# Kernel tuning notes

Hardware: AMD Instinct MI355X
Metric: run time of the kernel (lower is better)

The kernel has to match this reference:

```python
import jax, jax.numpy as jnp
import numpy as np

B, C, S = 2, 256, 24          # batch, hidden_size (channels), cube side
N = S * S * S                 # input_size = number of tokens (13824)
NH = 4                        # num_heads
DH = C // NH                  # head dim
P = 64                        # proj_size (low-rank K/V)
G = C // 32                   # conv groups in MHCResBlock
EPS_LN = 1e-5


def _lrelu(z):
    return jnp.where(z >= 0, z, 0.01 * z)


def _inorm(z):
    # instance norm over spatial dim, per (batch, channel); z: [B,C,N]
    m = jnp.mean(z, axis=-1, keepdims=True)
    v = jnp.var(z, axis=-1, keepdims=True)
    return (z - m) * jax.lax.rsqrt(v + EPS_LN)


def _gconv(z, w, b):
    # grouped 1x1x1 conv as per-group channel matmul; z: [B,C,N], w: [G,cin_g,cout_g]
    g, cin_g, cout_g = w.shape
    zg = z.reshape(z.shape[0], g, cin_g, z.shape[-1])
    out = jnp.einsum('bgin,gio->bgon', zg, w).reshape(z.shape[0], g * cout_g, z.shape[-1])
    return out + b[None, :, None]


def _ln(z, g, b):
    m = jnp.mean(z, axis=-1, keepdims=True)
    v = jnp.var(z, axis=-1, keepdims=True)
    return (z - m) * jax.lax.rsqrt(v + EPS_LN) * g + b


def _forward(x, pos_embed, ln_g, ln_b, gamma, temperature2, w_qkv, w_e, b_e,
             w_pool, b_pool, w_fc1, w_fc2, w_out1, b_out1, w_out2, b_out2,
             w_conv1, b_conv1, w_conv2, b_conv2):
    b_, c_, h_, w_, d_ = x.shape
    n_ = h_ * w_ * d_
    xf = x.reshape(b_, c_, n_)                      # [B,C,N]

    # MHCResBlock (UnetResBlock with grouped 1x1x1 convs + instance norm + lrelu)
    hdd = _lrelu(_inorm(_gconv(xf, w_conv1, b_conv1)))
    hdd = _inorm(_gconv(hdd, w_conv2, b_conv2))
    xc = _lrelu(hdd + xf)                           # [B,C,N]

    # tokens + pos embed + shared LayerNorm
    xt = xf.transpose(0, 2, 1) + pos_embed          # [B,N,C]
    xct = xc.transpose(0, 2, 1) + pos_embed
    x_n = _ln(xt, ln_g, ln_b)
    xc_n = _ln(xct, ln_g, ln_b)

    # QKV
    qkv = (x_n @ w_qkv).reshape(b_, n_, 3, NH, DH).transpose(2, 0, 3, 1, 4)  # [3,B,h,N,d]
    q, k, v = qkv[0], qkv[1], qkv[2]                # [B,h,N,d]
    qT = q.transpose(0, 1, 3, 2)                    # [B,h,d,N]
    kT = k.transpose(0, 1, 3, 2)
    vT = v.transpose(0, 1, 3, 2)

    # shared low-rank projection E == F over token dim (pre-normalization, as in source)
    k_proj = kT @ w_e + b_e                         # [B,h,d,P]
    v_proj = vT @ w_e + b_e                         # [B,h,d,P]

    # L2-normalize q over token dim (torch F.normalize eps=1e-12)
    qn = qT / jnp.maximum(jnp.linalg.norm(qT, axis=-1, keepdims=True), 1e-12)

    # channel attention: pool over tokens -> gated MLP -> sigmoid gate
    pooled = (xc_n.transpose(0, 2, 1) @ w_pool + b_pool).transpose(0, 2, 1)  # [B,1,C]
    gate = jax.nn.sigmoid(jax.nn.relu(pooled @ w_fc1) @ w_fc2)               # [B,1,C]
    x_CA = xc_n * gate                              # [B,N,C] (dropout = identity, eval)

    # spatial attention with projected K/V and per-head temperature
    attn = jnp.einsum('bhdn,bhdp->bhnp', qn, k_proj) * temperature2          # [B,h,N,P]
    attn = jax.nn.softmax(attn, axis=-1)
    x_SA = jnp.einsum('bhnp,bhdp->bhnd', attn, v_proj)                        # [B,h,N,d]
    # faithful permute(0,3,1,2).reshape(B,N,C) scramble from the source
    x_SA = x_SA.transpose(0, 3, 1, 2).reshape(b_, n_, c_)

    x_SA = x_SA @ w_out1 + b_out1                   # [B,N,C/2]
    x_CA = x_CA @ w_out2 + b_out2                   # [B,N,C/2]
    x_att = jnp.concatenate([x_SA, x_CA], axis=-1)  # [B,N,C]
    out = x_n + gamma * x_att
    return out.reshape(b_, h_, w_, d_, c_).transpose(0, 4, 1, 2, 3)


def setup_inputs() -> dict:
    key = jax.random.key(0)
    ks = jax.random.split(key, 16)
    f = lambda k, shape, sc=0.02: jax.random.normal(k, shape, jnp.float32) * sc
    return {
        'x': jax.random.normal(ks[0], (B, C, S, S, S), jnp.float32),
        'pos_embed': f(ks[1], (1, N, C)),
        'ln_g': jnp.ones((C,), jnp.float32),
        'ln_b': jnp.zeros((C,), jnp.float32),
        'gamma': jnp.full((C,), 1e-6, jnp.float32),
        'temperature2': jnp.ones((NH, 1, 1), jnp.float32),
        'w_qkv': f(ks[2], (C, 3 * C)),
        'w_e': f(ks[3], (N, P), 0.01),
        'b_e': jnp.zeros((P,), jnp.float32),
        'w_pool': f(ks[4], (N, 1), 0.01),
        'b_pool': jnp.zeros((1,), jnp.float32),
        'w_fc1': f(ks[5], (C, DH)),
        'w_fc2': f(ks[6], (DH, C)),
        'w_out1': f(ks[7], (C, C // 2)),
        'b_out1': jnp.zeros((C // 2,), jnp.float32),
        'w_out2': f(ks[8], (C, C // 2)),
        'b_out2': jnp.zeros((C // 2,), jnp.float32),
        'w_conv1': f(ks[9], (G, 32, 32), 0.1),
        'b_conv1': jnp.zeros((C,), jnp.float32),
        'w_conv2': f(ks[10], (G, 32, 32), 0.1),
        'b_conv2': jnp.zeros((C,), jnp.float32),
    }


def reference(x, pos_embed, ln_g, ln_b, gamma, temperature2, w_qkv, w_e, b_e,
              w_pool, b_pool, w_fc1, w_fc2, w_out1, b_out1, w_out2, b_out2,
              w_conv1, b_conv1, w_conv2, b_conv2):
    return _forward(x, pos_embed, ln_g, ln_b, gamma, temperature2, w_qkv, w_e, b_e,
                    w_pool, b_pool, w_fc1, w_fc2, w_out1, b_out1, w_out2, b_out2,
                    w_conv1, b_conv1, w_conv2, b_conv2)
```

## Files before the change

### kernel.cpp

```cpp
#include <hip/hip_runtime.h>
#include <hip/hip_bf16.h>
#include <math.h>

#define Bn 2
#define Cn 256
#define Nn 13824
#define NHn 4
#define Pn 64
#define Gn 8
#define NCH 54

typedef __bf16 bf16x8 __attribute__((ext_vector_type(8)));
typedef unsigned short us8v __attribute__((ext_vector_type(8)));
typedef unsigned short us4v __attribute__((ext_vector_type(4)));
typedef float f32x4 __attribute__((ext_vector_type(4)));

__device__ __forceinline__ unsigned short f2bf(float f) {
  __hip_bfloat16 h = __float2bfloat16(f);
  return __builtin_bit_cast(unsigned short, h);
}
__device__ __forceinline__ float bf2f(unsigned short u) {
  return __builtin_bit_cast(float, ((unsigned)u) << 16);
}
__device__ __forceinline__ unsigned pk2(float a, float b) {
  return (unsigned)f2bf(a) | ((unsigned)f2bf(b) << 16);
}

__global__ __launch_bounds__(256) void k_transpose_pos(const float* __restrict__ pos,
                                                       float* __restrict__ posT) {
  __shared__ float tile[64][65];
  int n0 = blockIdx.x * 64;
  int c0 = blockIdx.y * 64;
  int tc = threadIdx.x & 63;
  int tr = threadIdx.x >> 6;
  #pragma unroll
  for (int k = 0; k < 16; k++) {
    int n = tr + k * 4;
    tile[n][tc] = pos[(size_t)(n0 + n) * Cn + c0 + tc];
  }
  __syncthreads();
  #pragma unroll
  for (int k = 0; k < 16; k++) {
    int c = tr + k * 4;
    posT[(size_t)(c0 + c) * Nn + n0 + tc] = tile[tc][c];
  }
}

__global__ __launch_bounds__(256) void k_wcvt(const float* __restrict__ wqkv,
                                              const float* __restrict__ w1,
                                              unsigned short* __restrict__ wqT,
                                              unsigned short* __restrict__ w1T) {
  int j = blockIdx.x, c = threadIdx.x;
  if (j < 256) wqT[(size_t)j * 256 + c] = f2bf(wqkv[(size_t)c * 768 + j]);
  else w1T[(size_t)(j - 256) * 256 + c] = f2bf(w1[(size_t)c * 128 + (j - 256)]);
}

__global__ __launch_bounds__(256) void k_wet(const float* __restrict__ we,
                                             unsigned short* __restrict__ weT) {
  __shared__ float tile[64][65];
  int n0 = blockIdx.x * 64;
  int tc = threadIdx.x & 63;
  int tr = threadIdx.x >> 6;
  #pragma unroll
  for (int k = 0; k < 16; k++) {
    int n = tr + k * 4;
    tile[n][tc] = we[(size_t)(n0 + n) * Pn + tc];
  }
  __syncthreads();
  #pragma unroll
  for (int k = 0; k < 16; k++) {
    int p = tr + k * 4;
    weT[(size_t)p * Nn + n0 + tc] = f2bf(tile[tc][p]);
  }
}

template <bool NORM>
__global__ __launch_bounds__(256) void k_gconv(const float* __restrict__ src,
                                               const float* __restrict__ wt,
                                               const float* __restrict__ bias,
                                               const float* __restrict__ stats,
                                               float* __restrict__ dst,
                                               float* __restrict__ statacc) {
  int chunk = blockIdx.x, g = blockIdx.y, b = blockIdx.z;
  int t = threadIdx.x;
  int n = chunk * 256 + t;
  __shared__ float ws_[32][32];
  __shared__ float ms[32], rs[32], bs[32];
  __shared__ float sred[4][32][2];
  #pragma unroll
  for (int i = 0; i < 4; i++) {
    int e = t + 256 * i;
    ws_[e >> 5][e & 31] = wt[g * 1024 + e];
  }
  if (t < 32) {
    bs[t] = bias[g * 32 + t];
    if (NORM) {
      ms[t] = stats[(b * Cn + g * 32 + t) * 2 + 0];
      rs[t] = stats[(b * Cn + g * 32 + t) * 2 + 1];
    }
  }
  __syncthreads();
  float in[32];
  const float* sp = src + ((size_t)b * Cn + g * 32) * Nn + n;
  #pragma unroll
  for (int i = 0; i < 32; i++) {
    float v = sp[(size_t)i * Nn];
    if (NORM) {
      v = (v - ms[i]) * rs[i];
      v = v >= 0.f ? v : 0.01f * v;
    }
    in[i] = v;
  }
  int w = t >> 6, lane = t & 63;
  float* dp = dst + ((size_t)b * Cn + g * 32) * Nn + n;
  #pragma unroll
  for (int o = 0; o < 32; o++) {
    float acc = bs[o];
    #pragma unroll
    for (int i = 0; i < 32; i++) acc = fmaf(in[i], ws_[i][o], acc);
    dp[(size_t)o * Nn] = acc;
    float a = acc, a2 = acc * acc;
    #pragma unroll
    for (int off = 1; off < 64; off <<= 1) {
      a += __shfl_xor(a, off);
      a2 += __shfl_xor(a2, off);
    }
    if (lane == 0) { sred[w][o][0] = a; sred[w][o][1] = a2; }
  }
  __syncthreads();
  if (t < 64) {
    int o = t & 31, st = t >> 5;
    float v = sred[0][o][st] + sred[1][o][st] + sred[2][o][st] + sred[3][o][st];
    atomicAdd(&statacc[(b * Cn + g * 32 + o) * 2 + st], v);
  }
}

__global__ __launch_bounds__(256) void k_statfin(const float* __restrict__ acc,
                                                 float* __restrict__ stats) {
  int r = blockIdx.x * 256 + threadIdx.x;
  float s = acc[r * 2], ss = acc[r * 2 + 1];
  float m = s * (1.f / Nn);
  float var = ss * (1.f / Nn) - m * m;
  stats[r * 2 + 0] = m;
  stats[r * 2 + 1] = rsqrtf(var + 1e-5f);
}

__global__ __launch_bounds__(256) void k_fused_ln(
    const float* __restrict__ x, const float* __restrict__ t3,
    const float* __restrict__ posT, const float* __restrict__ stats3,
    const float* __restrict__ g, const float* __restrict__ beta,
    const float* __restrict__ wpool,
    unsigned short* __restrict__ xnbf, unsigned short* __restrict__ xnTbf,
    unsigned short* __restrict__ xcnbf, float* __restrict__ pooledacc) {
  int b = blockIdx.y, n0 = blockIdx.x * 32;
  int t = threadIdx.x, tg = t & 7, cg = t >> 3;
  int tok4 = tg * 4;
  __shared__ float vbuf[32 * 256];
  __shared__ float v2buf[32 * 256];
  __shared__ float red[4][8][4][4];
  __shared__ float tms[32][4];
  __shared__ float gb[256], bb[256], s3m[256], s3r[256];
  __shared__ float wp[32];
  __shared__ unsigned short Tb[2][32][36];

  gb[t] = g[t]; bb[t] = beta[t];
  s3m[t] = stats3[(b * Cn + t) * 2 + 0];
  s3r[t] = stats3[(b * Cn + t) * 2 + 1];
  if (t < 32) wp[t] = wpool[n0 + t];
  __syncthreads();

  float s1[4] = {}, q1[4] = {}, s2[4] = {}, q2[4] = {};
  #pragma unroll
  for (int ci = 0; ci < 8; ci++) {
    int c = ci * 32 + cg;
    f32x4 xv = *(const f32x4*)(x + ((size_t)b * Cn + c) * Nn + n0 + tok4);
    f32x4 pv = *(const f32x4*)(posT + (size_t)c * Nn + n0 + tok4);
    f32x4 tv = *(const f32x4*)(t3 + ((size_t)b * Cn + c) * Nn + n0 + tok4);
    float m3 = s3m[c], r3 = s3r[c];
    #pragma unroll
    for (int j = 0; j < 4; j++) {
      float v = xv[j] + pv[j];
      vbuf[(ci * 4 + j) * 256 + t] = v;
      s1[j] += v; q1[j] += v * v;
      float xcv = (tv[j] - m3) * r3 + xv[j];
      xcv = xcv >= 0.f ? xcv : 0.01f * xcv;
      float v2 = xcv + pv[j];
      v2buf[(ci * 4 + j) * 256 + t] = v2;
      s2[j] += v2; q2[j] += v2 * v2;
    }
  }
  #pragma unroll
  for (int j = 0; j < 4; j++) {
    float a = s1[j], bq = q1[j], c2 = s2[j], d2 = q2[j];
    #pragma unroll
    for (int off = 8; off < 64; off <<= 1) {
      a += __shfl_xor(a, off);
      bq += __shfl_xor(bq, off);
      c2 += __shfl_xor(c2, off);
      d2 += __shfl_xor(d2, off);
    }
    if ((t & 63) < 8) {
      int w = t >> 6, tgg = t & 7;
      red[w][tgg][j][0] = a; red[w][tgg][j][1] = bq;
      red[w][tgg][j][2] = c2; red[w][tgg][j][3] = d2;
    }
  }
  __syncthreads();
  if (t < 32) {
    int tgg = t >> 2, j = t & 3;
    float a = 0, bq = 0, c2 = 0, d2 = 0;
    #pragma unroll
    for (int w = 0; w < 4; w++) {
      a += red[w][tgg][j][0]; bq += red[w][tgg][j][1];
      c2 += red[w][tgg][j][2]; d2 += red[w][tgg][j][3];
    }
    float m1 = a * (1.f / 256.f);
    float r1 = rsqrtf(bq * (1.f / 256.f) - m1 * m1 + 1e-5f);
    float m2 = c2 * (1.f / 256.f);
    float r2 = rsqrtf(d2 * (1.f / 256.f) - m2 * m2 + 1e-5f);
    tms[t][0] = m1; tms[t][1] = r1; tms[t][2] = m2; tms[t][3] = r2;
  }
  __syncthreads();
  float m1v[4], r1v[4], m2v[4], r2v[4];
  #pragma unroll
  for (int j = 0; j < 4; j++) {
    m1v[j] = tms[tok4 + j][0]; r1v[j] = tms[tok4 + j][1];
    m2v[j] = tms[tok4 + j][2]; r2v[j] = tms[tok4 + j][3];
  }
  int row = t >> 3, seg = t & 7;
  #pragma unroll
  for (int ci = 0; ci < 8; ci++) {
    int c = ci * 32 + cg;
    float gg = gb[c], bv = bb[c];
    us4v o4;
    #pragma unroll
    for (int j = 0; j < 4; j++) {
      float v = vbuf[(ci * 4 + j) * 256 + t];
      o4[j] = f2bf((v - m1v[j]) * r1v[j] * gg + bv);
    }
    *(us4v*)(xnTbf + ((size_t)b * Cn + c) * Nn + n0 + tok4) = o4;
    #pragma unroll
    for (int j = 0; j < 4; j++) Tb[ci & 1][tok4 + j][cg] = o4[j];
    __syncthreads();
    *(us4v*)(xnbf + ((size_t)b * Nn + n0 + row) * Cn + ci * 32 + seg * 4) =
        *(const us4v*)&Tb[ci & 1][row][seg * 4];
  }
  #pragma unroll
  for (int ci = 0; ci < 8; ci++) {
    int c = ci * 32 + cg;
    float gg = gb[c], bv = bb[c];
    us4v o4;
    float pp = 0.f;
    #pragma unroll
    for (int j = 0; j < 4; j++) {
      float v = v2buf[(ci * 4 + j) * 256 + t];
      float o = (v - m2v[j]) * r2v[j] * gg + bv;
      o4[j] = f2bf(o);
      pp = fmaf(o, wp[tok4 + j], pp);
    }
    #pragma unroll
    for (int j = 0; j < 4; j++) Tb[ci & 1][tok4 + j][cg] = o4[j];
    pp += __shfl_xor(pp, 1);
    pp += __shfl_xor(pp, 2);
    pp += __shfl_xor(pp, 4);
    __syncthreads();
    *(us4v*)(xcnbf + ((size_t)b * Nn + n0 + row) * Cn + ci * 32 + seg * 4) =
        *(const us4v*)&Tb[ci & 1][row][seg * 4];
    if (tg == 0) atomicAdd(&pooledacc[b * Cn + c], pp);
  }
}

__global__ __launch_bounds__(256) void k_gemm_q(
    const unsigned short* __restrict__ Aw,
    const unsigned short* __restrict__ Bx,
    unsigned short* __restrict__ qo,
    float* __restrict__ qsq) {
  __shared__ char lds[24576];
  int b = blockIdx.z, n0 = blockIdx.x * 128, j0 = blockIdx.y * 64;
  int t = threadIdx.x, lane = t & 63, wid = t >> 6;
  int wj = wid >> 1, wt = wid & 1;
  f32x4 acc[2][4];
  #pragma unroll
  for (int i = 0; i < 2; i++)
    #pragma unroll
    for (int j = 0; j < 4; j++) acc[i][j] = (f32x4){0.f, 0.f, 0.f, 0.f};
  for (int k0 = 0; k0 < 256; k0 += 64) {
    {
      int r = t >> 2, off = (t & 3) * 16;
      const unsigned short* ga = Aw + (size_t)(j0 + r) * 256 + k0 + off;
      #pragma unroll
      for (int i = 0; i < 2; i++)
        *(us8v*)(lds + r * 128 + ((off * 2 + 16 * i) ^ ((r & 7) << 4))) = *(const us8v*)(ga + i * 8);
      int rb = t >> 1, offb = (t & 1) * 32;
      const unsigned short* gb = Bx + ((size_t)b * Nn + n0 + rb) * 256 + k0 + offb;
      #pragma unroll
      for (int i = 0; i < 4; i++)
        *(us8v*)(lds + 8192 + rb * 128 + ((offb * 2 + 16 * i) ^ ((rb & 7) << 4))) = *(const us8v*)(gb + i * 8);
    }
    __syncthreads();
    #pragma unroll
    for (int ks = 0; ks < 2; ks++) {
      int kb = ks * 64 + (lane >> 4) * 16;
      bf16x8 af[2], bfr[4];
      #pragma unroll
      for (int mt = 0; mt < 2; mt++) {
        int row = wj * 32 + mt * 16 + (lane & 15);
        af[mt] = *(bf16x8*)(lds + row * 128 + (kb ^ ((row & 7) << 4)));
      }
      #pragma unroll
      for (int tt = 0; tt < 4; tt++) {
        int row = wt * 64 + tt * 16 + (lane & 15);
        bfr[tt] = *(bf16x8*)(lds + 8192 + row * 128 + (kb ^ ((row & 7) << 4)));
      }
      #pragma unroll
      for (int mt = 0; mt < 2; mt++)
        #pragma unroll
        for (int tt = 0; tt < 4; tt++)
          acc[mt][tt] = __builtin_amdgcn_mfma_f32_16x16x32_bf16(af[mt], bfr[tt], acc[mt][tt], 0, 0, 0);
    }
    __syncthreads();
  }
  #pragma unroll
  for (int mt = 0; mt < 2; mt++)
    #pragma unroll
    for (int r = 0; r < 4; r++) {
      float v = 0.f;
      #pragma unroll
      for (int tt = 0; tt < 4; tt++) { float e = acc[mt][tt][r]; v = fmaf(e, e, v); }
      #pragma unroll
      for (int m = 1; m < 16; m <<= 1) v += __shfl_xor(v, m);
      if ((lane & 15) == 0)
        atomicAdd(&qsq[b * Cn + j0 + wj * 32 + mt * 16 + (lane >> 4) * 4 + r], v);
    }
  unsigned short* O = (unsigned short*)lds;
  #pragma unroll
  for (int mt = 0; mt < 2; mt++)
    #pragma unroll
    for (int tt = 0; tt < 4; tt++) {
      int tok = wt * 64 + tt * 16 + (lane & 15);
      int jb = wj * 32 + mt * 16 + ((lane >> 4) << 2);
      uint2 v;
      v.x = pk2(acc[mt][tt][0], acc[mt][tt][1]);
      v.y = pk2(acc[mt][tt][2], acc[mt][tt][3]);
      *(uint2*)(O + tok * 72 + jb) = v;
    }
  __syncthreads();
  int tok = t >> 1, js = (t & 1) * 32;
  unsigned short* dst = qo + ((size_t)b * Nn + n0 + tok) * 256 + j0 + js;
  #pragma unroll
  for (int i = 0; i < 4; i++) *(us8v*)(dst + i * 8) = *(const us8v*)(O + tok * 72 + js + i * 8);
}

__global__ __launch_bounds__(256) void k_xe(const unsigned short* __restrict__ xnT,
                                            const unsigned short* __restrict__ weT,
                                            float* __restrict__ part) {
  __shared__ char lds[16384];
  int chunk = blockIdx.x, ct = blockIdx.y, b = blockIdx.z;
  int c0 = ct * 64, nb = chunk * 256;
  int t = threadIdx.x, lane = t & 63, wid = t >> 6;
  f32x4 acc4[4];
  #pragma unroll
  for (int i = 0; i < 4; i++) acc4[i] = (f32x4){0.f, 0.f, 0.f, 0.f};
  for (int k0 = 0; k0 < 256; k0 += 64) {
    int r = t >> 2, off = (t & 3) * 16;
    const unsigned short* ga = xnT + ((size_t)b * Cn + c0 + r) * Nn + nb + k0 + off;
    const unsigned short* gb = weT + (size_t)r * Nn + nb + k0 + off;
    #pragma unroll
    for (int i = 0; i < 2; i++) {
      *(us8v*)(lds + r * 128 + ((off * 2 + 16 * i) ^ ((r & 7) << 4))) = *(const us8v*)(ga + i * 8);
      *(us8v*)(lds + 8192 + r * 128 + ((off * 2 + 16 * i) ^ ((r & 7) << 4))) = *(const us8v*)(gb + i * 8);
    }
    __syncthreads();
    #pragma unroll
    for (int ks = 0; ks < 2; ks++) {
      int kb = ks * 64 + (lane >> 4) * 16;
      int rowa = wid * 16 + (lane & 15);
      bf16x8 a = *(bf16x8*)(lds + rowa * 128 + (kb ^ ((rowa & 7) << 4)));
      #pragma unroll
      for (int pt = 0; pt < 4; pt++) {
        int rowb = pt * 16 + (lane & 15);
        bf16x8 bv = *(bf16x8*)(lds + 8192 + rowb * 128 + (kb ^ ((rowb & 7) << 4)));
        acc4[pt] = __builtin_amdgcn_mfma_f32_16x16x32_bf16(a, bv, acc4[pt], 0, 0, 0);
      }
    }
    __syncthreads();
  }
  size_t base = ((size_t)(b * NCH + chunk)) * (Cn * Pn);
  #pragma unroll
  for (int pt = 0; pt < 4; pt++)
    #pragma unroll
    for (int r = 0; r < 4; r++) {
      int c = c0 + wid * 16 + (lane >> 4) * 4 + r;
      int p = pt * 16 + (lane & 15);
      part[base + (size_t)c * Pn + p] = acc4[pt][r];
    }
}

__global__ __launch_bounds__(256) void k_xe_reduce(const float* __restrict__ part,
                                                   float* __restrict__ xe) {
  int i = blockIdx.x * 256 + threadIdx.x;
  int b = i / (Cn * Pn);
  int cp = i % (Cn * Pn);
  float s = 0.f;
  for (int ch = 0; ch < NCH; ch++) s += part[(size_t)(b * NCH + ch) * Cn * Pn + cp];
  xe[i] = s;
}

__global__ __launch_bounds__(256) void k_kvproj(const float* __restrict__ xe,
                                                const float* __restrict__ wqkv,
                                                const float* __restrict__ be,
                                                const float* __restrict__ qsq,
                                                const float* __restrict__ temp,
                                                unsigned short* __restrict__ kvp) {
  int hd = blockIdx.x * 4 + (threadIdx.x >> 6);
  int kv = blockIdx.y, b = blockIdx.z;
  int p = threadIdx.x & 63;
  int col = (kv + 1) * Cn + hd;
  float acc = be[p];
  for (int c = 0; c < Cn; c++)
    acc = fmaf(xe[((size_t)b * Cn + c) * Pn + p], wqkv[(size_t)c * 768 + col], acc);
  int h = hd >> 6, d = hd & 63;
  if (kv == 0) {
    float sc = 1.f / fmaxf(sqrtf(qsq[b * Cn + hd]), 1e-12f);
    acc *= sc * temp[h];
    kvp[((size_t)(b * 4 + h)) * 4096 + p * 64 + d] = f2bf(acc);
  } else {
    kvp[32768 + ((size_t)(b * 4 + h)) * 4096 + d * 64 + p] = f2bf(acc);
  }
}

__global__ __launch_bounds__(256) void k_gate(const float* __restrict__ pooledacc,
                                              const float* __restrict__ bpool,
                                              const float* __restrict__ wfc1,
                                              const float* __restrict__ wfc2,
                                              float* __restrict__ gate) {
  int b = blockIdx.x, t = threadIdx.x;
  __shared__ float pl[256], h1[64];
  pl[t] = pooledacc[b * Cn + t] + bpool[0];
  __syncthreads();
  if (t < 64) {
    float a = 0.f;
    for (int c = 0; c < Cn; c++) a = fmaf(pl[c], wfc1[c * 64 + t], a);
    h1[t] = fmaxf(a, 0.f);
  }
  __syncthreads();
  float a = 0.f;
  for (int j = 0; j < 64; j++) a = fmaf(h1[j], wfc2[j * Cn + t], a);
  gate[b * Cn + t] = 1.f / (1.f + __expf(-a));
}

__global__ __launch_bounds__(256) void k_w2gT(const float* __restrict__ gate,
                                              const float* __restrict__ w2,
                                              unsigned short* __restrict__ w2gT) {
  int j = blockIdx.x, b = blockIdx.y, c = threadIdx.x;
  w2gT[((size_t)b * 128 + j) * 256 + c] = f2bf(gate[b * Cn + c] * w2[(size_t)c * 128 + j]);
}

__global__ __launch_bounds__(128) void k_attn(const unsigned short* __restrict__ qbf,
                                              const unsigned short* __restrict__ kvp,
                                              unsigned short* __restrict__ xsa) {
  __shared__ char lds[16384 + 2 * 9216];
  int nb = blockIdx.x, h = blockIdx.y, b = blockIdx.z;
  int t = threadIdx.x, lane = t & 63, w = t >> 6;
  char* kpT = lds;
  char* vp = lds + 8192;
  unsigned short* P = (unsigned short*)(lds + 16384 + w * 9216);
  const unsigned short* kg = kvp + ((size_t)(b * 4 + h)) * 4096;
  const unsigned short* vg = kvp + 32768 + ((size_t)(b * 4 + h)) * 4096;
  {
    int r = t >> 1, off = (t & 1) * 32;
    #pragma unroll
    for (int i = 0; i < 4; i++) {
      *(us8v*)(kpT + r * 128 + ((off * 2 + 16 * i) ^ ((r & 7) << 4))) = *(const us8v*)(kg + r * 64 + off + i * 8);
      *(us8v*)(vp + r * 128 + ((off * 2 + 16 * i) ^ ((r & 7) << 4))) = *(const us8v*)(vg + r * 64 + off + i * 8);
    }
  }
  __syncthreads();
  int n0 = nb * 128 + w * 64;
  bf16x8 qf[4][2];
  #pragma unroll
  for (int tt = 0; tt < 4; tt++)
    #pragma unroll
    for (int ks = 0; ks < 2; ks++) {
      int n = n0 + tt * 16 + (lane & 15);
      qf[tt][ks] = *(const bf16x8*)(qbf + ((size_t)b * Nn + n) * 256 + h * 64 + ks * 32 + (lane >> 4) * 8);
    }
  f32x4 s[4][4];
  #pragma unroll
  for (int i = 0; i < 4; i++)
    #pragma unroll
    for (int j = 0; j < 4; j++) s[i][j] = (f32x4){0.f, 0.f, 0.f, 0.f};
  #pragma unroll
  for (int ks = 0; ks < 2; ks++) {
    int kb = ks * 64 + (lane >> 4) * 16;
    #pragma unroll
    for (int mt = 0; mt < 4; mt++) {
      int row = mt * 16 + (lane & 15);
      bf16x8 a = *(bf16x8*)(kpT + row * 128 + (kb ^ ((row & 7) << 4)));
      #pragma unroll
      for (int tt = 0; tt < 4; tt++)
        s[mt][tt] = __builtin_amdgcn_mfma_f32_16x16x32_bf16(a, qf[tt][ks], s[mt][tt], 0, 0, 0);
    }
  }
  #pragma unroll
  for (int tt = 0; tt < 4; tt++) {
    float mx = -1e30f;
    #pragma unroll
    for (int mt = 0; mt < 4; mt++)
      #pragma unroll
      for (int r = 0; r < 4; r++) mx = fmaxf(mx, s[mt][tt][r]);
    mx = fmaxf(mx, __shfl_xor(mx, 16));
    mx = fmaxf(mx, __shfl_xor(mx, 32));
    float den = 0.f;
    #pragma unroll
    for (int mt = 0; mt < 4; mt++)
      #pragma unroll
      for (int r = 0; r < 4; r++) {
        float e = __expf(s[mt][tt][r] - mx);
        s[mt][tt][r] = e; den += e;
      }
    den += __shfl_xor(den, 16);
    den += __shfl_xor(den, 32);
    float inv = 1.f / den;
    #pragma unroll
    for (int mt = 0; mt < 4; mt++)
      #pragma unroll
      for (int r = 0; r < 4; r++) s[mt][tt][r] *= inv;
  }
  #pragma unroll
  for (int mt = 0; mt < 4; mt++)
    #pragma unroll
    for (int tt = 0; tt < 4; tt++) {
      int tok = tt * 16 + (lane & 15);
      int pb = mt * 16 + ((lane >> 4) << 2);
      uint2 v;
      v.x = pk2(s[mt][tt][0], s[mt][tt][1]);
      v.y = pk2(s[mt][tt][2], s[mt][tt][3]);
      *(uint2*)(P + tok * 72 + pb) = v;
    }
  bf16x8 pf[4][2];
  #pragma unroll
  for (int mt = 0; mt < 4; mt++)
    #pragma unroll
    for (int ks = 0; ks < 2; ks++)
      pf[mt][ks] = *(const bf16x8*)(P + (mt * 16 + (lane & 15)) * 72 + ks * 32 + (lane >> 4) * 8);
  f32x4 o[4][4];
  #pragma unroll
  for (int i = 0; i < 4; i++)
    #pragma unroll
    for (int j = 0; j < 4; j++) o[i][j] = (f32x4){0.f, 0.f, 0.f, 0.f};
  #pragma unroll
  for (int ks = 0; ks < 2; ks++) {
    int kb = ks * 64 + (lane >> 4) * 16;
    #pragma unroll
    for (int nt = 0; nt < 4; nt++) {
      int row = nt * 16 + (lane & 15);
      bf16x8 bfv = *(bf16x8*)(vp + row * 128 + (kb ^ ((row & 7) << 4)));
      #pragma unroll
      for (int mt = 0; mt < 4; mt++)
        o[mt][nt] = __builtin_amdgcn_mfma_f32_16x16x32_bf16(pf[mt][ks], bfv, o[mt][nt], 0, 0, 0);
    }
  }
  #pragma unroll
  for (int mt = 0; mt < 4; mt++)
    #pragma unroll
    for (int nt = 0; nt < 4; nt++) {
      int d = nt * 16 + (lane & 15);
      int tb = mt * 16 + ((lane >> 4) << 2);
      uint2 v;
      v.x = pk2(o[mt][nt][0], o[mt][nt][1]);
      v.y = pk2(o[mt][nt][2], o[mt][nt][3]);
      *(uint2*)(P + d * 72 + tb) = v;
    }
  size_t fb = (size_t)b * Cn * Nn + ((size_t)(lane * 4 + h)) * Nn + n0;
  #pragma unroll
  for (int k = 0; k < 8; k++)
    *(us8v*)(xsa + fb + k * 8) = *(const us8v*)(P + lane * 72 + k * 8);
}

__global__ __launch_bounds__(256) void k_gemm_out(
    const unsigned short* __restrict__ Aw, size_t a_bstride,
    const unsigned short* __restrict__ Bx,
    const float* __restrict__ bias, int cbase,
    const unsigned short* __restrict__ xnT, const float* __restrict__ gamma,
    float* __restrict__ outp) {
  __shared__ char lds[33792];
  int b = blockIdx.z, n0 = blockIdx.x * 128, j0 = blockIdx.y * 64;
  int t = threadIdx.x, lane = t & 63, wid = t >> 6;
  int wj = wid >> 1, wt = wid & 1;
  const unsigned short* Ab = Aw + a_bstride * b;
  f32x4 acc[2][4];
  #pragma unroll
  for (int i = 0; i < 2; i++)
    #pragma unroll
    for (int j = 0; j < 4; j++) acc[i][j] = (f32x4){0.f, 0.f, 0.f, 0.f};
  for (int k0 = 0; k0 < 256; k0 += 64) {
    {
      int r = t >> 2, off = (t & 3) * 16;
      const unsigned short* ga = Ab + (size_t)(j0 + r) * 256 + k0 + off;
      #pragma unroll
      for (int i = 0; i < 2; i++)
        *(us8v*)(lds + r * 128 + ((off * 2 + 16 * i) ^ ((r & 7) << 4))) = *(const us8v*)(ga + i * 8);
      int rb = t >> 1, offb = (t & 1) * 32;
      const unsigned short* gb = Bx + ((size_t)b * Nn + n0 + rb) * 256 + k0 + offb;
      #pragma unroll
      for (int i = 0; i < 4; i++)
        *(us8v*)(lds + 8192 + rb * 128 + ((offb * 2 + 16 * i) ^ ((rb & 7) << 4))) = *(const us8v*)(gb + i * 8);
    }
    __syncthreads();
    #pragma unroll
    for (int ks = 0; ks < 2; ks++) {
      int kb = ks * 64 + (lane >> 4) * 16;
      bf16x8 af[2], bfr[4];
      #pragma unroll
      for (int mt = 0; mt < 2; mt++) {
        int row = wj * 32 + mt * 16 + (lane & 15);
        af[mt] = *(bf16x8*)(lds + row * 128 + (kb ^ ((row & 7) << 4)));
      }
      #pragma unroll
      for (int tt = 0; tt < 4; tt++) {
        int row = wt * 64 + tt * 16 + (lane & 15);
        bfr[tt] = *(bf16x8*)(lds + 8192 + row * 128 + (kb ^ ((row & 7) << 4)));
      }
      #pragma unroll
      for (int mt = 0; mt < 2; mt++)
        #pragma unroll
        for (int tt = 0; tt < 4; tt++)
          acc[mt][tt] = __builtin_amdgcn_mfma_f32_16x16x32_bf16(af[mt], bfr[tt], acc[mt][tt], 0, 0, 0);
    }
    __syncthreads();
  }
  float* OT = (float*)lds;
  #pragma unroll
  for (int mt = 0; mt < 2; mt++)
    #pragma unroll
    for (int tt = 0; tt < 4; tt++)
      #pragma unroll
      for (int r = 0; r < 4; r++) {
        int j = wj * 32 + mt * 16 + (lane >> 4) * 4 + r;
        int tok = wt * 64 + tt * 16 + (lane & 15);
        OT[j * 132 + tok] = acc[mt][tt][r];
      }
  __syncthreads();
  int jj = t >> 2, ts = (t & 3) * 32;
  int c = cbase + j0 + jj;
  float gm = gamma[c], bi = bias[j0 + jj];
  const unsigned short* xn = xnT + ((size_t)b * Cn + c) * Nn + n0 + ts;
  float* op = outp + ((size_t)b * Cn + c) * Nn + n0 + ts;
  #pragma unroll
  for (int i = 0; i < 8; i++) {
    f32x4 v = *(const f32x4*)(&OT[jj * 132 + ts + i * 4]);
    us4v xv = *(const us4v*)(xn + i * 4);
    f32x4 ov;
    #pragma unroll
    for (int e = 0; e < 4; e++) ov[e] = bf2f(xv[e]) + gm * (v[e] + bi);
    *(f32x4*)(op + i * 4) = ov;
  }
}

extern "C" void kernel_launch(void* const* d_in, const int* in_sizes, int n_in,
                              void* d_out, int out_size, void* d_ws, size_t ws_size,
                              hipStream_t stream) {
  const float* x      = (const float*)d_in[0];
  const float* pos    = (const float*)d_in[1];
  const float* ln_g   = (const float*)d_in[2];
  const float* ln_b   = (const float*)d_in[3];
  const float* gamma  = (const float*)d_in[4];
  const float* temp2  = (const float*)d_in[5];
  const float* w_qkv  = (const float*)d_in[6];
  const float* w_e    = (const float*)d_in[7];
  const float* b_e    = (const float*)d_in[8];
  const float* w_pool = (const float*)d_in[9];
  const float* b_pool = (const float*)d_in[10];
  const float* w_fc1  = (const float*)d_in[11];
  const float* w_fc2  = (const float*)d_in[12];
  const float* w_out1 = (const float*)d_in[13];
  const float* b_out1 = (const float*)d_in[14];
  const float* w_out2 = (const float*)d_in[15];
  const float* b_out2 = (const float*)d_in[16];
  const float* w_c1   = (const float*)d_in[17];
  const float* b_c1   = (const float*)d_in[18];
  const float* w_c2   = (const float*)d_in[19];
  const float* b_c2   = (const float*)d_in[20];
  (void)in_sizes; (void)n_in; (void)out_size; (void)ws_size;
  float* out = (float*)d_out;

  const size_t SZ = (size_t)Bn * Cn * Nn;
  const size_t NC = (size_t)Nn * Cn;
  char* base = (char*)d_ws;
  size_t off = 0;
  auto alloc = [&](size_t bytes) { void* p = base + off; off += (bytes + 255) & ~(size_t)255; return p; };
  float* t3     = (float*)alloc(SZ * 4);
  char*  alias  = (char*)alloc(SZ * 4);
  float* posT   = (float*)alloc(NC * 4);
  float* xepart = (float*)alloc((size_t)NCH * Bn * Cn * Pn * 4);
  unsigned short* xnbf  = (unsigned short*)alloc(SZ * 2);
  unsigned short* xnTbf = (unsigned short*)alloc(SZ * 2);
  unsigned short* xcnbf = (unsigned short*)alloc(SZ * 2);
  unsigned short* weT   = (unsigned short*)alloc((size_t)Pn * Nn * 2);
  float* zeros  = (float*)alloc(3072 * 4);
  float* stats1acc = zeros;
  float* stats3acc = zeros + 1024;
  float* qsq       = zeros + 2048;
  float* pooledacc = zeros + 2560;
  float* stats1 = (float*)alloc(1024 * 4);
  float* stats3 = (float*)alloc(1024 * 4);
  float* xe     = (float*)alloc(32768 * 4);
  float* gateb  = (float*)alloc(512 * 4);
  unsigned short* kvp  = (unsigned short*)alloc(65536 * 2);
  unsigned short* w2gt = (unsigned short*)alloc(65536 * 2);
  unsigned short* wqT  = (unsigned short*)alloc(65536 * 2);
  unsigned short* w1T  = (unsigned short*)alloc(32768 * 2);

  float* t1 = (float*)alias;
  unsigned short* qbf   = (unsigned short*)alias;
  unsigned short* xsabf = (unsigned short*)alias + SZ;

  hipMemsetAsync(zeros, 0, 3072 * 4, stream);
  k_wcvt<<<dim3(384), 256, 0, stream>>>(w_qkv, w_out1, wqT, w1T);
  k_wet<<<dim3(216), 256, 0, stream>>>(w_e, weT);
  k_transpose_pos<<<dim3(216, 4), 256, 0, stream>>>(pos, posT);
  k_gconv<false><<<dim3(NCH, Gn, Bn), 256, 0, stream>>>(x, w_c1, b_c1, nullptr, t1, stats1acc);
  k_statfin<<<dim3(2), 256, 0, stream>>>(stats1acc, stats1);
  k_gconv<true><<<dim3(NCH, Gn, Bn), 256, 0, stream>>>(t1, w_c2, b_c2, stats1, t3, stats3acc);
  k_statfin<<<dim3(2), 256, 0, stream>>>(stats3acc, stats3);
  k_fused_ln<<<dim3(432, Bn), 256, 0, stream>>>(x, t3, posT, stats3, ln_g, ln_b, w_pool,
                                                xnbf, xnTbf, xcnbf, pooledacc);
  k_gemm_q<<<dim3(108, 4, Bn), 256, 0, stream>>>(wqT, xnbf, qbf, qsq);
  k_xe<<<dim3(NCH, 4, Bn), 256, 0, stream>>>(xnTbf, weT, xepart);
  k_xe_reduce<<<dim3(128), 256, 0, stream>>>(xepart, xe);
  k_kvproj<<<dim3(64, 2, Bn), 256, 0, stream>>>(xe, w_qkv, b_e, qsq, temp2, kvp);
  k_gate<<<dim3(Bn), 256, 0, stream>>>(pooledacc, b_pool, w_fc1, w_fc2, gateb);
  k_w2gT<<<dim3(128, Bn), 256, 0, stream>>>(gateb, w_out2, w2gt);
  k_attn<<<dim3(108, NHn, Bn), 128, 0, stream>>>(qbf, kvp, xsabf);
  k_gemm_out<<<dim3(108, 2, Bn), 256, 0, stream>>>(w1T, 0, xsabf, b_out1, 0, xnTbf, gamma, out);
  k_gemm_out<<<dim3(108, 2, Bn), 256, 0, stream>>>(w2gt, (size_t)128 * 256, xcnbf, b_out2, 128, xnTbf, gamma, out);
}
```

Baseline: 406.6 us.

## Move grouped convs to bf16 MFMA GEMMs on token-major layout and merge prep kernels

Replaces the scalar FP32 grouped 1x1x1 convolutions with a generic bf16 MFMA GEMM kernel that uses block-diagonal expanded weights on a token-major bf16 copy of x. Intermediates become bf16, and the instance-norm statistics are accumulated in the GEMM epilogue. All weight conversions, the input transpose and the zeroing are merged into a single prep kernel. LayerNorm is rewritten to read token-major bf16, a separate transpose produces xnT, and the gate is applied inside the output GEMM rather than prebuilt. This cuts FP32 memory traffic and launch count, at the cost of dense 256x256 matmuls that waste 7/8 of their FLOPs on zero blocks and lower-precision intermediates.

```diff
diff --git a/kernel.cpp b/kernel.cpp
--- a/kernel.cpp
+++ b/kernel.cpp
@@ -26,113 +26,235 @@
   return (unsigned)f2bf(a) | ((unsigned)f2bf(b) << 16);
 }
 
-__global__ __launch_bounds__(256) void k_transpose_pos(const float* __restrict__ pos,
-                                                       float* __restrict__ posT) {
-  __shared__ float tile[64][65];
-  int n0 = blockIdx.x * 64;
-  int c0 = blockIdx.y * 64;
-  int tc = threadIdx.x & 63;
-  int tr = threadIdx.x >> 6;
-  #pragma unroll
-  for (int k = 0; k < 16; k++) {
-    int n = tr + k * 4;
-    tile[n][tc] = pos[(size_t)(n0 + n) * Cn + c0 + tc];
-  }
-  __syncthreads();
-  #pragma unroll
-  for (int k = 0; k < 16; k++) {
-    int c = tr + k * 4;
-    posT[(size_t)(c0 + c) * Nn + n0 + tc] = tile[tc][c];
-  }
-}
-
-__global__ __launch_bounds__(256) void k_wcvt(const float* __restrict__ wqkv,
-                                              const float* __restrict__ w1,
-                                              unsigned short* __restrict__ wqT,
-                                              unsigned short* __restrict__ w1T) {
-  int j = blockIdx.x, c = threadIdx.x;
-  if (j < 256) wqT[(size_t)j * 256 + c] = f2bf(wqkv[(size_t)c * 768 + j]);
-  else w1T[(size_t)(j - 256) * 256 + c] = f2bf(w1[(size_t)c * 128 + (j - 256)]);
-}
-
-__global__ __launch_bounds__(256) void k_wet(const float* __restrict__ we,
-                                             unsigned short* __restrict__ weT) {
-  __shared__ float tile[64][65];
-  int n0 = blockIdx.x * 64;
-  int tc = threadIdx.x & 63;
-  int tr = threadIdx.x >> 6;
-  #pragma unroll
-  for (int k = 0; k < 16; k++) {
-    int n = tr + k * 4;
-    tile[n][tc] = we[(size_t)(n0 + n) * Pn + tc];
-  }
-  __syncthreads();
-  #pragma unroll
-  for (int k = 0; k < 16; k++) {
-    int p = tr + k * 4;
-    weT[(size_t)p * Nn + n0 + tc] = f2bf(tile[tc][p]);
-  }
-}
-
-template <bool NORM>
-__global__ __launch_bounds__(256) void k_gconv(const float* __restrict__ src,
-                                               const float* __restrict__ wt,
-                                               const float* __restrict__ bias,
-                                               const float* __restrict__ stats,
-                                               float* __restrict__ dst,
-                                               float* __restrict__ statacc) {
-  int chunk = blockIdx.x, g = blockIdx.y, b = blockIdx.z;
-  int t = threadIdx.x;
-  int n = chunk * 256 + t;
-  __shared__ float ws_[32][32];
-  __shared__ float ms[32], rs[32], bs[32];
-  __shared__ float sred[4][32][2];
-  #pragma unroll
-  for (int i = 0; i < 4; i++) {
-    int e = t + 256 * i;
-    ws_[e >> 5][e & 31] = wt[g * 1024 + e];
-  }
-  if (t < 32) {
-    bs[t] = bias[g * 32 + t];
-    if (NORM) {
-      ms[t] = stats[(b * Cn + g * 32 + t) * 2 + 0];
-      rs[t] = stats[(b * Cn + g * 32 + t) * 2 + 1];
-    }
-  }
-  __syncthreads();
-  float in[32];
-  const float* sp = src + ((size_t)b * Cn + g * 32) * Nn + n;
-  #pragma unroll
-  for (int i = 0; i < 32; i++) {
-    float v = sp[(size_t)i * Nn];
-    if (NORM) {
-      v = (v - ms[i]) * rs[i];
-      v = v >= 0.f ? v : 0.01f * v;
-    }
-    in[i] = v;
-  }
-  int w = t >> 6, lane = t & 63;
-  float* dp = dst + ((size_t)b * Cn + g * 32) * Nn + n;
-  #pragma unroll
-  for (int o = 0; o < 32; o++) {
-    float acc = bs[o];
-    #pragma unroll
-    for (int i = 0; i < 32; i++) acc = fmaf(in[i], ws_[i][o], acc);
-    dp[(size_t)o * Nn] = acc;
-    float a = acc, a2 = acc * acc;
-    #pragma unroll
-    for (int off = 1; off < 64; off <<= 1) {
-      a += __shfl_xor(a, off);
-      a2 += __shfl_xor(a2, off);
-    }
-    if (lane == 0) { sred[w][o][0] = a; sred[w][o][1] = a2; }
-  }
-  __syncthreads();
-  if (t < 64) {
-    int o = t & 31, st = t >> 5;
-    float v = sred[0][o][st] + sred[1][o][st] + sred[2][o][st] + sred[3][o][st];
-    atomicAdd(&statacc[(b * Cn + g * 32 + o) * 2 + st], v);
-  }
+__global__ __launch_bounds__(256) void k_prep(
+    const float* __restrict__ x, const float* __restrict__ wqkv,
+    const float* __restrict__ w_e, const float* __restrict__ w1,
+    const float* __restrict__ w2, const float* __restrict__ wc1,
+    const float* __restrict__ wc2,
+    unsigned short* __restrict__ xTbf, unsigned short* __restrict__ W1e,
+    unsigned short* __restrict__ W2e, unsigned short* __restrict__ wqkvT,
+    unsigned short* __restrict__ w1T, unsigned short* __restrict__ w2T,
+    unsigned short* __restrict__ weT, float* __restrict__ zeros) {
+  __shared__ float tl[64][65];
+  int bid = blockIdx.x, t = threadIdx.x;
+  if (bid == 0) {
+    #pragma unroll
+    for (int i = 0; i < 12; i++) zeros[t + i * 256] = 0.f;
+    return;
+  }
+  bid -= 1;
+  if (bid < 1728) {
+    int b = bid / 864, rem = bid % 864;
+    int c0 = (rem / 216) * 64, n0 = (rem % 216) * 64;
+    int nc = t & 63, cr = t >> 6;
+    #pragma unroll
+    for (int k = 0; k < 16; k++)
+      tl[cr + k * 4][nc] = x[((size_t)b * Cn + c0 + cr + k * 4) * Nn + n0 + nc];
+    __syncthreads();
+    int nrow = t >> 2, cs = (t & 3) * 16;
+    us8v o0, o1;
+    #pragma unroll
+    for (int i = 0; i < 8; i++) {
+      o0[i] = f2bf(tl[cs + i][nrow]);
+      o1[i] = f2bf(tl[cs + 8 + i][nrow]);
+    }
+    unsigned short* dp = xTbf + ((size_t)b * Nn + n0 + nrow) * 256 + c0 + cs;
+    *(us8v*)dp = o0; *(us8v*)(dp + 8) = o1;
+    return;
+  }
+  bid -= 1728;
+  if (bid < 512) {
+    int cv = bid >> 8, cout = bid & 255, cin = t;
+    const float* w = cv ? wc2 : wc1;
+    unsigned short* We = cv ? W2e : W1e;
+    float val = ((cout >> 5) == (cin >> 5))
+                    ? w[(cout >> 5) * 1024 + (cin & 31) * 32 + (cout & 31)] : 0.f;
+    We[cout * 256 + cin] = f2bf(val);
+    return;
+  }
+  bid -= 512;
+  if (bid < 48) {
+    int j0 = (bid / 4) * 64, c0 = (bid & 3) * 64;
+    int jc = t & 63, cr = t >> 6;
+    #pragma unroll
+    for (int k = 0; k < 16; k++)
+      tl[cr + k * 4][jc] = wqkv[(size_t)(c0 + cr + k * 4) * 768 + j0 + jc];
+    __syncthreads();
+    int jrow = t >> 2, cs = (t & 3) * 16;
+    us8v o0, o1;
+    #pragma unroll
+    for (int i = 0; i < 8; i++) {
+      o0[i] = f2bf(tl[cs + i][jrow]);
+      o1[i] = f2bf(tl[cs + 8 + i][jrow]);
+    }
+    unsigned short* dp = wqkvT + (size_t)(j0 + jrow) * 256 + c0 + cs;
+    *(us8v*)dp = o0; *(us8v*)(dp + 8) = o1;
+    return;
+  }
+  bid -= 48;
+  if (bid < 16) {
+    int mat = bid >> 3, rem = bid & 7;
+    int j0 = (rem >> 2) * 64, c0 = (rem & 3) * 64;
+    const float* src = mat ? w2 : w1;
+    unsigned short* dstw = mat ? w2T : w1T;
+    int jc = t & 63, cr = t >> 6;
+    #pragma unroll
+    for (int k = 0; k < 16; k++)
+      tl[cr + k * 4][jc] = src[(size_t)(c0 + cr + k * 4) * 128 + j0 + jc];
+    __syncthreads();
+    int jrow = t >> 2, cs = (t & 3) * 16;
+    us8v o0, o1;
+    #pragma unroll
+    for (int i = 0; i < 8; i++) {
+      o0[i] = f2bf(tl[cs + i][jrow]);
+      o1[i] = f2bf(tl[cs + 8 + i][jrow]);
+    }
+    unsigned short* dp = dstw + (size_t)(j0 + jrow) * 256 + c0 + cs;
+    *(us8v*)dp = o0; *(us8v*)(dp + 8) = o1;
+    return;
+  }
+  bid -= 16;
+  {
+    int n0 = bid * 64;
+    int p = t & 63, nr = t >> 6;
+    #pragma unroll
+    for (int k = 0; k < 16; k++)
+      tl[nr + k * 4][p] = w_e[(size_t)(n0 + nr + k * 4) * 64 + p];
+    __syncthreads();
+    int prow = t >> 2, ns = (t & 3) * 16;
+    us8v o0, o1;
+    #pragma unroll
+    for (int i = 0; i < 8; i++) {
+      o0[i] = f2bf(tl[ns + i][prow]);
+      o1[i] = f2bf(tl[ns + 8 + i][prow]);
+    }
+    unsigned short* dp = weT + (size_t)prow * Nn + n0 + ns;
+    *(us8v*)dp = o0; *(us8v*)(dp + 8) = o1;
+  }
+}
+
+template <int MODE>
+__global__ __launch_bounds__(256) void k_mm(
+    const unsigned short* __restrict__ Aw, const unsigned short* __restrict__ Bx,
+    const float* __restrict__ bias, const float* __restrict__ instats,
+    unsigned short* __restrict__ dst, float* __restrict__ statacc) {
+  __shared__ char lds[36864];
+  int b = blockIdx.z, n0 = blockIdx.x * 128, j0 = blockIdx.y * 128;
+  int t = threadIdx.x, lane = t & 63, wid = t >> 6;
+  int wj = wid >> 1, wt = wid & 1;
+  float* bias_s = (float*)(lds + 33792);
+  float* ms = (float*)(lds + 34304);
+  float* rs = (float*)(lds + 35328);
+  if (MODE != 2 && t < 128) bias_s[t] = bias[j0 + t];
+  if (MODE == 1) {
+    ms[t] = instats[(b * Cn + t) * 2 + 0];
+    rs[t] = instats[(b * Cn + t) * 2 + 1];
+  }
+  __syncthreads();
+  f32x4 acc[4][4];
+  #pragma unroll
+  for (int i = 0; i < 4; i++)
+    #pragma unroll
+    for (int j = 0; j < 4; j++) acc[i][j] = (f32x4){0.f, 0.f, 0.f, 0.f};
+  int r = t >> 1, off = (t & 1) * 32;
+  for (int k0 = 0; k0 < 256; k0 += 64) {
+    const unsigned short* ga = Aw + (size_t)(j0 + r) * 256 + k0 + off;
+    const unsigned short* gb = Bx + ((size_t)b * Nn + n0 + r) * 256 + k0 + off;
+    #pragma unroll
+    for (int i = 0; i < 4; i++) {
+      *(us8v*)(lds + r * 128 + ((off * 2 + 16 * i) ^ ((r & 7) << 4))) = *(const us8v*)(ga + i * 8);
+      us8v v = *(const us8v*)(gb + i * 8);
+      if (MODE == 1) {
+        #pragma unroll
+        for (int e = 0; e < 8; e++) {
+          int c = k0 + off + i * 8 + e;
+          float f = (bf2f(v[e]) - ms[c]) * rs[c];
+          f = f >= 0.f ? f : 0.01f * f;
+          v[e] = f2bf(f);
+        }
+      }
+      *(us8v*)(lds + 16384 + r * 128 + ((off * 2 + 16 * i) ^ ((r & 7) << 4))) = v;
+    }
+    __syncthreads();
+    #pragma unroll
+    for (int ks = 0; ks < 2; ks++) {
+      int kb = ks * 64 + (lane >> 4) * 16;
+      bf16x8 af[4], bfr[4];
+      #pragma unroll
+      for (int mt = 0; mt < 4; mt++) {
+        int row = wj * 64 + mt * 16 + (lane & 15);
+        af[mt] = *(bf16x8*)(lds + row * 128 + (kb ^ ((row & 7) << 4)));
+      }
+      #pragma unroll
+      for (int tt = 0; tt < 4; tt++) {
+        int row = wt * 64 + tt * 16 + (lane & 15);
+        bfr[tt] = *(bf16x8*)(lds + 16384 + row * 128 + (kb ^ ((row & 7) << 4)));
+      }
+      #pragma unroll
+      for (int mt = 0; mt < 4; mt++)
+        #pragma unroll
+        for (int tt = 0; tt < 4; tt++)
+          acc[mt][tt] = __builtin_amdgcn_mfma_f32_16x16x32_bf16(af[mt], bfr[tt], acc[mt][tt], 0, 0, 0);
+    }
+    __syncthreads();
+  }
+  if (MODE != 2) {
+    #pragma unroll
+    for (int mt = 0; mt < 4; mt++)
+      #pragma unroll
+      for (int tt = 0; tt < 4; tt++)
+        #pragma unroll
+        for (int e = 0; e < 4; e++)
+          acc[mt][tt][e] += bias_s[wj * 64 + mt * 16 + (lane >> 4) * 4 + e];
+    #pragma unroll
+    for (int mt = 0; mt < 4; mt++)
+      #pragma unroll
+      for (int e = 0; e < 4; e++) {
+        float s = 0.f, ss = 0.f;
+        #pragma unroll
+        for (int tt = 0; tt < 4; tt++) {
+          float v = acc[mt][tt][e];
+          s += v; ss = fmaf(v, v, ss);
+        }
+        #pragma unroll
+        for (int m = 1; m < 16; m <<= 1) { s += __shfl_xor(s, m); ss += __shfl_xor(ss, m); }
+        if ((lane & 15) == 0) {
+          int c = b * Cn + j0 + wj * 64 + mt * 16 + (lane >> 4) * 4 + e;
+          atomicAdd(&statacc[c * 2 + 0], s);
+          atomicAdd(&statacc[c * 2 + 1], ss);
+        }
+      }
+  } else {
+    #pragma unroll
+    for (int mt = 0; mt < 4; mt++)
+      #pragma unroll
+      for (int e = 0; e < 4; e++) {
+        float ss = 0.f;
+        #pragma unroll
+        for (int tt = 0; tt < 4; tt++) { float v = acc[mt][tt][e]; ss = fmaf(v, v, ss); }
+        #pragma unroll
+        for (int m = 1; m < 16; m <<= 1) ss += __shfl_xor(ss, m);
+        if ((lane & 15) == 0)
+          atomicAdd(&statacc[b * Cn + j0 + wj * 64 + mt * 16 + (lane >> 4) * 4 + e], ss);
+      }
+  }
+  unsigned short* O = (unsigned short*)lds;
+  #pragma unroll
+  for (int mt = 0; mt < 4; mt++)
+    #pragma unroll
+    for (int tt = 0; tt < 4; tt++) {
+      int tok = wt * 64 + tt * 16 + (lane & 15);
+      int jb = wj * 64 + mt * 16 + (lane >> 4) * 4;
+      uint2 v;
+      v.x = pk2(acc[mt][tt][0], acc[mt][tt][1]);
+      v.y = pk2(acc[mt][tt][2], acc[mt][tt][3]);
+      *(uint2*)(O + tok * 132 + jb) = v;
+    }
+  __syncthreads();
+  int tok = t >> 1, js = (t & 1) * 64;
+  unsigned short* dp = dst + ((size_t)b * Nn + n0 + tok) * 256 + j0 + js;
+  #pragma unroll
+  for (int i = 0; i < 8; i++) *(us8v*)(dp + i * 8) = *(const us8v*)(O + tok * 132 + js + i * 8);
 }
 
 __global__ __launch_bounds__(256) void k_statfin(const float* __restrict__ acc,
@@ -146,209 +268,114 @@
 }
 
 __global__ __launch_bounds__(256) void k_fused_ln(
-    const float* __restrict__ x, const float* __restrict__ t3,
-    const float* __restrict__ posT, const float* __restrict__ stats3,
+    const unsigned short* __restrict__ xT, const unsigned short* __restrict__ t3T,
+    const float* __restrict__ pos, const float* __restrict__ stats3,
     const float* __restrict__ g, const float* __restrict__ beta,
     const float* __restrict__ wpool,
-    unsigned short* __restrict__ xnbf, unsigned short* __restrict__ xnTbf,
-    unsigned short* __restrict__ xcnbf, float* __restrict__ pooledacc) {
+    unsigned short* __restrict__ xnbf, unsigned short* __restrict__ xcnbf,
+    float* __restrict__ pooledacc) {
   int b = blockIdx.y, n0 = blockIdx.x * 32;
-  int t = threadIdx.x, tg = t & 7, cg = t >> 3;
-  int tok4 = tg * 4;
-  __shared__ float vbuf[32 * 256];
-  __shared__ float v2buf[32 * 256];
-  __shared__ float red[4][8][4][4];
-  __shared__ float tms[32][4];
-  __shared__ float gb[256], bb[256], s3m[256], s3r[256];
-  __shared__ float wp[32];
-  __shared__ unsigned short Tb[2][32][36];
-
-  gb[t] = g[t]; bb[t] = beta[t];
+  int t = threadIdx.x;
+  int tokid = t >> 3, cseg = t & 7;
+  __shared__ float s3m[256], s3r[256], gb[256], bb[256];
+  __shared__ float pred[4][8][32];
   s3m[t] = stats3[(b * Cn + t) * 2 + 0];
   s3r[t] = stats3[(b * Cn + t) * 2 + 1];
-  if (t < 32) wp[t] = wpool[n0 + t];
-  __syncthreads();
-
-  float s1[4] = {}, q1[4] = {}, s2[4] = {}, q2[4] = {};
-  #pragma unroll
-  for (int ci = 0; ci < 8; ci++) {
-    int c = ci * 32 + cg;
-    f32x4 xv = *(const f32x4*)(x + ((size_t)b * Cn + c) * Nn + n0 + tok4);
-    f32x4 pv = *(const f32x4*)(posT + (size_t)c * Nn + n0 + tok4);
-    f32x4 tv = *(const f32x4*)(t3 + ((size_t)b * Cn + c) * Nn + n0 + tok4);
-    float m3 = s3m[c], r3 = s3r[c];
-    #pragma unroll
-    for (int j = 0; j < 4; j++) {
-      float v = xv[j] + pv[j];
-      vbuf[(ci * 4 + j) * 256 + t] = v;
-      s1[j] += v; q1[j] += v * v;
-      float xcv = (tv[j] - m3) * r3 + xv[j];
-      xcv = xcv >= 0.f ? xcv : 0.01f * xcv;
-      float v2 = xcv + pv[j];
-      v2buf[(ci * 4 + j) * 256 + t] = v2;
-      s2[j] += v2; q2[j] += v2 * v2;
-    }
-  }
-  #pragma unroll
-  for (int j = 0; j < 4; j++) {
-    float a = s1[j], bq = q1[j], c2 = s2[j], d2 = q2[j];
-    #pragma unroll
-    for (int off = 8; off < 64; off <<= 1) {
-      a += __shfl_xor(a, off);
-      bq += __shfl_xor(bq, off);
-      c2 += __shfl_xor(c2, off);
-      d2 += __shfl_xor(d2, off);
-    }
-    if ((t & 63) < 8) {
-      int w = t >> 6, tgg = t & 7;
-      red[w][tgg][j][0] = a; red[w][tgg][j][1] = bq;
-      red[w][tgg][j][2] = c2; red[w][tgg][j][3] = d2;
-    }
-  }
-  __syncthreads();
-  if (t < 32) {
-    int tgg = t >> 2, j = t & 3;
-    float a = 0, bq = 0, c2 = 0, d2 = 0;
-    #pragma unroll
-    for (int w = 0; w < 4; w++) {
-      a += red[w][tgg][j][0]; bq += red[w][tgg][j][1];
-      c2 += red[w][tgg][j][2]; d2 += red[w][tgg][j][3];
-    }
-    float m1 = a * (1.f / 256.f);
-    float r1 = rsqrtf(bq * (1.f / 256.f) - m1 * m1 + 1e-5f);
-    float m2 = c2 * (1.f / 256.f);
-    float r2 = rsqrtf(d2 * (1.f / 256.f) - m2 * m2 + 1e-5f);
-    tms[t][0] = m1; tms[t][1] = r1; tms[t][2] = m2; tms[t][3] = r2;
-  }
-  __syncthreads();
-  float m1v[4], r1v[4], m2v[4], r2v[4];
-  #pragma unroll
-  for (int j = 0; j < 4; j++) {
-    m1v[j] = tms[tok4 + j][0]; r1v[j] = tms[tok4 + j][1];
-    m2v[j] = tms[tok4 + j][2]; r2v[j] = tms[tok4 + j][3];
-  }
-  int row = t >> 3, seg = t & 7;
-  #pragma unroll
-  for (int ci = 0; ci < 8; ci++) {
-    int c = ci * 32 + cg;
-    float gg = gb[c], bv = bb[c];
-    us4v o4;
-    #pragma unroll
-    for (int j = 0; j < 4; j++) {
-      float v = vbuf[(ci * 4 + j) * 256 + t];
-      o4[j] = f2bf((v - m1v[j]) * r1v[j] * gg + bv);
-    }
-    *(us4v*)(xnTbf + ((size_t)b * Cn + c) * Nn + n0 + tok4) = o4;
-    #pragma unroll
-    for (int j = 0; j < 4; j++) Tb[ci & 1][tok4 + j][cg] = o4[j];
-    __syncthreads();
-    *(us4v*)(xnbf + ((size_t)b * Nn + n0 + row) * Cn + ci * 32 + seg * 4) =
-        *(const us4v*)&Tb[ci & 1][row][seg * 4];
-  }
-  #pragma unroll
-  for (int ci = 0; ci < 8; ci++) {
-    int c = ci * 32 + cg;
-    float gg = gb[c], bv = bb[c];
-    us4v o4;
-    float pp = 0.f;
-    #pragma unroll
-    for (int j = 0; j < 4; j++) {
-      float v = v2buf[(ci * 4 + j) * 256 + t];
-      float o = (v - m2v[j]) * r2v[j] * gg + bv;
-      o4[j] = f2bf(o);
-      pp = fmaf(o, wp[tok4 + j], pp);
-    }
-    #pragma unroll
-    for (int j = 0; j < 4; j++) Tb[ci & 1][tok4 + j][cg] = o4[j];
-    pp += __shfl_xor(pp, 1);
-    pp += __shfl_xor(pp, 2);
-    pp += __shfl_xor(pp, 4);
-    __syncthreads();
-    *(us4v*)(xcnbf + ((size_t)b * Nn + n0 + row) * Cn + ci * 32 + seg * 4) =
-        *(const us4v*)&Tb[ci & 1][row][seg * 4];
-    if (tg == 0) atomicAdd(&pooledacc[b * Cn + c], pp);
-  }
-}
-
-__global__ __launch_bounds__(256) void k_gemm_q(
-    const unsigned short* __restrict__ Aw,
-    const unsigned short* __restrict__ Bx,
-    unsigned short* __restrict__ qo,
-    float* __restrict__ qsq) {
-  __shared__ char lds[24576];
-  int b = blockIdx.z, n0 = blockIdx.x * 128, j0 = blockIdx.y * 64;
-  int t = threadIdx.x, lane = t & 63, wid = t >> 6;
-  int wj = wid >> 1, wt = wid & 1;
-  f32x4 acc[2][4];
-  #pragma unroll
-  for (int i = 0; i < 2; i++)
-    #pragma unroll
-    for (int j = 0; j < 4; j++) acc[i][j] = (f32x4){0.f, 0.f, 0.f, 0.f};
-  for (int k0 = 0; k0 < 256; k0 += 64) {
-    {
-      int r = t >> 2, off = (t & 3) * 16;
-      const unsigned short* ga = Aw + (size_t)(j0 + r) * 256 + k0 + off;
-      #pragma unroll
-      for (int i = 0; i < 2; i++)
-        *(us8v*)(lds + r * 128 + ((off * 2 + 16 * i) ^ ((r & 7) << 4))) = *(const us8v*)(ga + i * 8);
-      int rb = t >> 1, offb = (t & 1) * 32;
-      const unsigned short* gb = Bx + ((size_t)b * Nn + n0 + rb) * 256 + k0 + offb;
-      #pragma unroll
-      for (int i = 0; i < 4; i++)
-        *(us8v*)(lds + 8192 + rb * 128 + ((offb * 2 + 16 * i) ^ ((rb & 7) << 4))) = *(const us8v*)(gb + i * 8);
-    }
-    __syncthreads();
-    #pragma unroll
-    for (int ks = 0; ks < 2; ks++) {
-      int kb = ks * 64 + (lane >> 4) * 16;
-      bf16x8 af[2], bfr[4];
-      #pragma unroll
-      for (int mt = 0; mt < 2; mt++) {
-        int row = wj * 32 + mt * 16 + (lane & 15);
-        af[mt] = *(bf16x8*)(lds + row * 128 + (kb ^ ((row & 7) << 4)));
-      }
-      #pragma unroll
-      for (int tt = 0; tt < 4; tt++) {
-        int row = wt * 64 + tt * 16 + (lane & 15);
-        bfr[tt] = *(bf16x8*)(lds + 8192 + row * 128 + (kb ^ ((row & 7) << 4)));
-      }
-      #pragma unroll
-      for (int mt = 0; mt < 2; mt++)
-        #pragma unroll
-        for (int tt = 0; tt < 4; tt++)
-          acc[mt][tt] = __builtin_amdgcn_mfma_f32_16x16x32_bf16(af[mt], bfr[tt], acc[mt][tt], 0, 0, 0);
-    }
-    __syncthreads();
-  }
-  #pragma unroll
-  for (int mt = 0; mt < 2; mt++)
-    #pragma unroll
-    for (int r = 0; r < 4; r++) {
-      float v = 0.f;
-      #pragma unroll
-      for (int tt = 0; tt < 4; tt++) { float e = acc[mt][tt][r]; v = fmaf(e, e, v); }
-      #pragma unroll
-      for (int m = 1; m < 16; m <<= 1) v += __shfl_xor(v, m);
-      if ((lane & 15) == 0)
-        atomicAdd(&qsq[b * Cn + j0 + wj * 32 + mt * 16 + (lane >> 4) * 4 + r], v);
-    }
-  unsigned short* O = (unsigned short*)lds;
-  #pragma unroll
-  for (int mt = 0; mt < 2; mt++)
-    #pragma unroll
-    for (int tt = 0; tt < 4; tt++) {
-      int tok = wt * 64 + tt * 16 + (lane & 15);
-      int jb = wj * 32 + mt * 16 + ((lane >> 4) << 2);
-      uint2 v;
-      v.x = pk2(acc[mt][tt][0], acc[mt][tt][1]);
-      v.y = pk2(acc[mt][tt][2], acc[mt][tt][3]);
-      *(uint2*)(O + tok * 72 + jb) = v;
-    }
-  __syncthreads();
-  int tok = t >> 1, js = (t & 1) * 32;
-  unsigned short* dst = qo + ((size_t)b * Nn + n0 + tok) * 256 + j0 + js;
-  #pragma unroll
-  for (int i = 0; i < 4; i++) *(us8v*)(dst + i * 8) = *(const us8v*)(O + tok * 72 + js + i * 8);
+  gb[t] = g[t]; bb[t] = beta[t];
+  __syncthreads();
+  int n = n0 + tokid;
+  size_t rowb = ((size_t)b * Nn + n) * 256 + cseg * 32;
+  size_t rowp = (size_t)n * 256 + cseg * 32;
+  float v1[32], v2[32];
+  float s1 = 0.f, q1 = 0.f, s2 = 0.f, q2 = 0.f;
+  #pragma unroll
+  for (int i = 0; i < 4; i++) {
+    us8v x8 = *(const us8v*)(xT + rowb + i * 8);
+    us8v t8 = *(const us8v*)(t3T + rowb + i * 8);
+    f32x4 pa = *(const f32x4*)(pos + rowp + i * 8);
+    f32x4 pb = *(const f32x4*)(pos + rowp + i * 8 + 4);
+    #pragma unroll
+    for (int j = 0; j < 8; j++) {
+      int c = cseg * 32 + i * 8 + j;
+      float xv = bf2f(x8[j]);
+      float pv = j < 4 ? pa[j] : pb[j - 4];
+      float a = xv + pv;
+      v1[i * 8 + j] = a;
+      s1 += a; q1 = fmaf(a, a, q1);
+      float xc = (bf2f(t8[j]) - s3m[c]) * s3r[c] + xv;
+      xc = xc >= 0.f ? xc : 0.01f * xc;
+      float d = xc + pv;
+      v2[i * 8 + j] = d;
+      s2 += d; q2 = fmaf(d, d, q2);
+    }
+  }
+  #pragma unroll
+  for (int m = 1; m < 8; m <<= 1) {
+    s1 += __shfl_xor(s1, m); q1 += __shfl_xor(q1, m);
+    s2 += __shfl_xor(s2, m); q2 += __shfl_xor(q2, m);
+  }
+  float m1 = s1 * (1.f / 256.f);
+  float r1 = rsqrtf(q1 * (1.f / 256.f) - m1 * m1 + 1e-5f);
+  float m2 = s2 * (1.f / 256.f);
+  float r2 = rsqrtf(q2 * (1.f / 256.f) - m2 * m2 + 1e-5f);
+  float wpl = wpool[n];
+  float pp[32];
+  #pragma unroll
+  for (int i = 0; i < 4; i++) {
+    us8v o1, o2;
+    #pragma unroll
+    for (int j = 0; j < 8; j++) {
+      int c = cseg * 32 + i * 8 + j;
+      o1[j] = f2bf((v1[i * 8 + j] - m1) * r1 * gb[c] + bb[c]);
+      float oc = (v2[i * 8 + j] - m2) * r2 * gb[c] + bb[c];
+      o2[j] = f2bf(oc);
+      pp[i * 8 + j] = oc * wpl;
+    }
+    *(us8v*)(xnbf + rowb + i * 8) = o1;
+    *(us8v*)(xcnbf + rowb + i * 8) = o2;
+  }
+  #pragma unroll
+  for (int i = 0; i < 32; i++) {
+    pp[i] += __shfl_xor(pp[i], 8);
+    pp[i] += __shfl_xor(pp[i], 16);
+    pp[i] += __shfl_xor(pp[i], 32);
+  }
+  int w = t >> 6;
+  if ((t & 63) < 8) {
+    #pragma unroll
+    for (int i = 0; i < 32; i++) pred[w][t & 7][i] = pp[i];
+  }
+  __syncthreads();
+  float psum = pred[0][t >> 5][t & 31] + pred[1][t >> 5][t & 31] +
+               pred[2][t >> 5][t & 31] + pred[3][t >> 5][t & 31];
+  atomicAdd(&pooledacc[b * Cn + t], psum);
+}
+
+__global__ __launch_bounds__(256) void k_xpose(const unsigned short* __restrict__ src,
+                                               unsigned short* __restrict__ dstT) {
+  __shared__ unsigned tile[64][33];
+  int n0 = blockIdx.x * 64, c0 = blockIdx.y * 64, b = blockIdx.z;
+  int t = threadIdx.x;
+  int nr = t >> 2, cs = (t & 3) * 16;
+  const unsigned short* sp = src + ((size_t)b * Nn + n0 + nr) * 256 + c0 + cs;
+  us8v v0 = *(const us8v*)sp;
+  us8v v1 = *(const us8v*)(sp + 8);
+  unsigned* tp = &tile[nr][cs >> 1];
+  #pragma unroll
+  for (int i = 0; i < 4; i++) tp[i] = (unsigned)v0[2 * i] | ((unsigned)v0[2 * i + 1] << 16);
+  #pragma unroll
+  for (int i = 0; i < 4; i++) tp[4 + i] = (unsigned)v1[2 * i] | ((unsigned)v1[2 * i + 1] << 16);
+  __syncthreads();
+  int crow = t >> 2, ns = (t & 3) * 16;
+  int c2 = crow >> 1, sel = (crow & 1) * 16;
+  us8v o0, o1;
+  #pragma unroll
+  for (int i = 0; i < 8; i++) {
+    o0[i] = (unsigned short)(tile[ns + i][c2] >> sel);
+    o1[i] = (unsigned short)(tile[ns + 8 + i][c2] >> sel);
+  }
+  unsigned short* dp = dstT + ((size_t)b * Cn + c0 + crow) * Nn + n0 + ns;
+  *(us8v*)dp = o0; *(us8v*)(dp + 8) = o1;
 }
 
 __global__ __launch_bounds__(256) void k_xe(const unsigned short* __restrict__ xnT,
@@ -389,10 +416,10 @@
   #pragma unroll
   for (int pt = 0; pt < 4; pt++)
     #pragma unroll
-    for (int r = 0; r < 4; r++) {
-      int c = c0 + wid * 16 + (lane >> 4) * 4 + r;
+    for (int e = 0; e < 4; e++) {
+      int c = c0 + wid * 16 + (lane >> 4) * 4 + e;
       int p = pt * 16 + (lane & 15);
-      part[base + (size_t)c * Pn + p] = acc4[pt][r];
+      part[base + (size_t)c * Pn + p] = acc4[pt][e];
     }
 }
 
@@ -449,13 +476,6 @@
   gate[b * Cn + t] = 1.f / (1.f + __expf(-a));
 }
 
-__global__ __launch_bounds__(256) void k_w2gT(const float* __restrict__ gate,
-                                              const float* __restrict__ w2,
-                                              unsigned short* __restrict__ w2gT) {
-  int j = blockIdx.x, b = blockIdx.y, c = threadIdx.x;
-  w2gT[((size_t)b * 128 + j) * 256 + c] = f2bf(gate[b * Cn + c] * w2[(size_t)c * 128 + j]);
-}
-
 __global__ __launch_bounds__(128) void k_attn(const unsigned short* __restrict__ qbf,
                                               const unsigned short* __restrict__ kvp,
                                               unsigned short* __restrict__ xsa) {
@@ -508,16 +528,16 @@
     #pragma unroll
     for (int mt = 0; mt < 4; mt++)
       #pragma unroll
-      for (int r = 0; r < 4; r++) mx = fmaxf(mx, s[mt][tt][r]);
+      for (int e = 0; e < 4; e++) mx = fmaxf(mx, s[mt][tt][e]);
     mx = fmaxf(mx, __shfl_xor(mx, 16));
     mx = fmaxf(mx, __shfl_xor(mx, 32));
     float den = 0.f;
     #pragma unroll
     for (int mt = 0; mt < 4; mt++)
       #pragma unroll
-      for (int r = 0; r < 4; r++) {
-        float e = __expf(s[mt][tt][r] - mx);
-        s[mt][tt][r] = e; den += e;
+      for (int e = 0; e < 4; e++) {
+        float ev = __expf(s[mt][tt][e] - mx);
+        s[mt][tt][e] = ev; den += ev;
       }
     den += __shfl_xor(den, 16);
     den += __shfl_xor(den, 32);
@@ -525,7 +545,7 @@
     #pragma unroll
     for (int mt = 0; mt < 4; mt++)
       #pragma unroll
-      for (int r = 0; r < 4; r++) s[mt][tt][r] *= inv;
+      for (int e = 0; e < 4; e++) s[mt][tt][e] *= inv;
   }
   #pragma unroll
   for (int mt = 0; mt < 4; mt++)
@@ -578,17 +598,21 @@
     *(us8v*)(xsa + fb + k * 8) = *(const us8v*)(P + lane * 72 + k * 8);
 }
 
+template <int GATE>
 __global__ __launch_bounds__(256) void k_gemm_out(
-    const unsigned short* __restrict__ Aw, size_t a_bstride,
+    const unsigned short* __restrict__ Aw,
     const unsigned short* __restrict__ Bx,
     const float* __restrict__ bias, int cbase,
     const unsigned short* __restrict__ xnT, const float* __restrict__ gamma,
+    const float* __restrict__ gate,
     float* __restrict__ outp) {
-  __shared__ char lds[33792];
+  __shared__ char lds[34816];
   int b = blockIdx.z, n0 = blockIdx.x * 128, j0 = blockIdx.y * 64;
   int t = threadIdx.x, lane = t & 63, wid = t >> 6;
   int wj = wid >> 1, wt = wid & 1;
-  const unsigned short* Ab = Aw + a_bstride * b;
+  float* gs = (float*)(lds + 33792);
+  if (GATE) { gs[t] = gate[b * Cn + t]; }
+  __syncthreads();
   f32x4 acc[2][4];
   #pragma unroll
   for (int i = 0; i < 2; i++)
@@ -597,15 +621,21 @@
   for (int k0 = 0; k0 < 256; k0 += 64) {
     {
       int r = t >> 2, off = (t & 3) * 16;
-      const unsigned short* ga = Ab + (size_t)(j0 + r) * 256 + k0 + off;
-      #pragma unroll
-      for (int i = 0; i < 2; i++)
-        *(us8v*)(lds + r * 128 + ((off * 2 + 16 * i) ^ ((r & 7) << 4))) = *(const us8v*)(ga + i * 8);
+      const unsigned short* ga = Aw + (size_t)(j0 + r) * 256 + k0 + off;
+      #pragma unroll
+      for (int i = 0; i < 2; i++) {
+        us8v v = *(const us8v*)(ga + i * 8);
+        if (GATE) {
+          #pragma unroll
+          for (int e = 0; e < 8; e++) v[e] = f2bf(bf2f(v[e]) * gs[k0 + off + i * 8 + e]);
+        }
+        *(us8v*)(lds + r * 128 + ((off * 2 + 16 * i) ^ ((r & 7) << 4))) = v;
+      }
       int rb = t >> 1, offb = (t & 1) * 32;
-      const unsigned short* gb = Bx + ((size_t)b * Nn + n0 + rb) * 256 + k0 + offb;
+      const unsigned short* gbp = Bx + ((size_t)b * Nn + n0 + rb) * 256 + k0 + offb;
       #pragma unroll
       for (int i = 0; i < 4; i++)
-        *(us8v*)(lds + 8192 + rb * 128 + ((offb * 2 + 16 * i) ^ ((rb & 7) << 4))) = *(const us8v*)(gb + i * 8);
+        *(us8v*)(lds + 8192 + rb * 128 + ((offb * 2 + 16 * i) ^ ((rb & 7) << 4))) = *(const us8v*)(gbp + i * 8);
     }
     __syncthreads();
     #pragma unroll
@@ -636,10 +666,10 @@
     #pragma unroll
     for (int tt = 0; tt < 4; tt++)
       #pragma unroll
-      for (int r = 0; r < 4; r++) {
-        int j = wj * 32 + mt * 16 + (lane >> 4) * 4 + r;
+      for (int e = 0; e < 4; e++) {
+        int j = wj * 32 + mt * 16 + (lane >> 4) * 4 + e;
         int tok = wt * 64 + tt * 16 + (lane & 15);
-        OT[j * 132 + tok] = acc[mt][tt][r];
+        OT[j * 132 + tok] = acc[mt][tt][e];
       }
   __syncthreads();
   int jj = t >> 2, ts = (t & 3) * 32;
@@ -686,18 +716,23 @@
   float* out = (float*)d_out;
 
   const size_t SZ = (size_t)Bn * Cn * Nn;
-  const size_t NC = (size_t)Nn * Cn;
   char* base = (char*)d_ws;
   size_t off = 0;
   auto alloc = [&](size_t bytes) { void* p = base + off; off += (bytes + 255) & ~(size_t)255; return p; };
-  float* t3     = (float*)alloc(SZ * 4);
-  char*  alias  = (char*)alloc(SZ * 4);
-  float* posT   = (float*)alloc(NC * 4);
+  unsigned short* xTbf  = (unsigned short*)alloc(SZ * 2);
+  unsigned short* t1T   = (unsigned short*)alloc(SZ * 2);
+  unsigned short* t3T   = (unsigned short*)alloc(SZ * 2);
+  unsigned short* xnbf  = (unsigned short*)alloc(SZ * 2);
+  unsigned short* xcnbf = (unsigned short*)alloc(SZ * 2);
+  unsigned short* xnTbf = (unsigned short*)alloc(SZ * 2);
+  unsigned short* xsabf = (unsigned short*)alloc(SZ * 2);
+  unsigned short* W1e   = (unsigned short*)alloc(65536 * 2);
+  unsigned short* W2e   = (unsigned short*)alloc(65536 * 2);
+  unsigned short* wqkvT = (unsigned short*)alloc((size_t)768 * 256 * 2);
+  unsigned short* w1T   = (unsigned short*)alloc(32768 * 2);
+  unsigned short* w2T   = (unsigned short*)alloc(32768 * 2);
+  unsigned short* weT   = (unsigned short*)alloc((size_t)Pn * Nn * 2);
   float* xepart = (float*)alloc((size_t)NCH * Bn * Cn * Pn * 4);
-  unsigned short* xnbf  = (unsigned short*)alloc(SZ * 2);
-  unsigned short* xnTbf = (unsigned short*)alloc(SZ * 2);
-  unsigned short* xcnbf = (unsigned short*)alloc(SZ * 2);
-  unsigned short* weT   = (unsigned short*)alloc((size_t)Pn * Nn * 2);
   float* zeros  = (float*)alloc(3072 * 4);
   float* stats1acc = zeros;
   float* stats3acc = zeros + 1024;
@@ -707,32 +742,24 @@
   float* stats3 = (float*)alloc(1024 * 4);
   float* xe     = (float*)alloc(32768 * 4);
   float* gateb  = (float*)alloc(512 * 4);
-  unsigned short* kvp  = (unsigned short*)alloc(65536 * 2);
-  unsigned short* w2gt = (unsigned short*)alloc(65536 * 2);
-  unsigned short* wqT  = (unsigned short*)alloc(65536 * 2);
-  unsigned short* w1T  = (unsigned short*)alloc(32768 * 2);
-
-  float* t1 = (float*)alias;
-  unsigned short* qbf   = (unsigned short*)alias;
-  unsigned short* xsabf = (unsigned short*)alias + SZ;
-
-  hipMemsetAsync(zeros, 0, 3072 * 4, stream);
-  k_wcvt<<<dim3(384), 256, 0, stream>>>(w_qkv, w_out1, wqT, w1T);
-  k_wet<<<dim3(216), 256, 0, stream>>>(w_e, weT);
-  k_transpose_pos<<<dim3(216, 4), 256, 0, stream>>>(pos, posT);
-  k_gconv<false><<<dim3(NCH, Gn, Bn), 256, 0, stream>>>(x, w_c1, b_c1, nullptr, t1, stats1acc);
+  unsigned short* kvp = (unsigned short*)alloc(65536 * 2);
+  unsigned short* qbf = t1T;
+
+  k_prep<<<dim3(2521), 256, 0, stream>>>(x, w_qkv, w_e, w_out1, w_out2, w_c1, w_c2,
+                                         xTbf, W1e, W2e, wqkvT, w1T, w2T, weT, zeros);
+  k_mm<0><<<dim3(108, 2, Bn), 256, 0, stream>>>(W1e, xTbf, b_c1, nullptr, t1T, stats1acc);
   k_statfin<<<dim3(2), 256, 0, stream>>>(stats1acc, stats1);
-  k_gconv<true><<<dim3(NCH, Gn, Bn), 256, 0, stream>>>(t1, w_c2, b_c2, stats1, t3, stats3acc);
+  k_mm<1><<<dim3(108, 2, Bn), 256, 0, stream>>>(W2e, t1T, b_c2, stats1, t3T, stats3acc);
   k_statfin<<<dim3(2), 256, 0, stream>>>(stats3acc, stats3);
-  k_fused_ln<<<dim3(432, Bn), 256, 0, stream>>>(x, t3, posT, stats3, ln_g, ln_b, w_pool,
-                                                xnbf, xnTbf, xcnbf, pooledacc);
-  k_gemm_q<<<dim3(108, 4, Bn), 256, 0, stream>>>(wqT, xnbf, qbf, qsq);
+  k_fused_ln<<<dim3(432, Bn), 256, 0, stream>>>(xTbf, t3T, pos, stats3, ln_g, ln_b,
+                                                w_pool, xnbf, xcnbf, pooledacc);
+  k_mm<2><<<dim3(108, 2, Bn), 256, 0, stream>>>(wqkvT, xnbf, nullptr, nullptr, qbf, qsq);
+  k_xpose<<<dim3(216, 4, Bn), 256, 0, stream>>>(xnbf, xnTbf);
   k_xe<<<dim3(NCH, 4, Bn), 256, 0, stream>>>(xnTbf, weT, xepart);
   k_xe_reduce<<<dim3(128), 256, 0, stream>>>(xepart, xe);
   k_kvproj<<<dim3(64, 2, Bn), 256, 0, stream>>>(xe, w_qkv, b_e, qsq, temp2, kvp);
   k_gate<<<dim3(Bn), 256, 0, stream>>>(pooledacc, b_pool, w_fc1, w_fc2, gateb);
-  k_w2gT<<<dim3(128, Bn), 256, 0, stream>>>(gateb, w_out2, w2gt);
   k_attn<<<dim3(108, NHn, Bn), 128, 0, stream>>>(qbf, kvp, xsabf);
-  k_gemm_out<<<dim3(108, 2, Bn), 256, 0, stream>>>(w1T, 0, xsabf, b_out1, 0, xnTbf, gamma, out);
-  k_gemm_out<<<dim3(108, 2, Bn), 256, 0, stream>>>(w2gt, (size_t)128 * 256, xcnbf, b_out2, 128, xnTbf, gamma, out);
-}
+  k_gemm_out<0><<<dim3(108, 2, Bn), 256, 0, stream>>>(w1T, xsabf, b_out1, 0, xnTbf, gamma, nullptr, out);
+  k_gemm_out<1><<<dim3(108, 2, Bn), 256, 0, stream>>>(w2T, xcnbf, b_out2, 128, xnTbf, gamma, gateb, out);
+}
```

After: 424.9 us. 1.05x slower.
